# Optimization experiments

Hardware: AMD Instinct MI355X
Metric: run time of the kernel (lower is better)

The kernel has to match this reference:

```python
import jax, jax.numpy as jnp
import numpy as np

B, N, F_IN, F_OUT = 1, 8192, 256, 256
ALPHA = 0.2  # leaky relu negative slope
NEG_INF = -9e15


def setup_inputs() -> dict:
    key = jax.random.key(0)
    ks = jax.random.split(key, 8)
    feat = jax.random.normal(ks[0], (B, N, F_IN), dtype=jnp.float32)
    adj = jax.random.randint(ks[1], (B, N, N), 0, 2, dtype=jnp.int32)
    s = 1.414 * (6.0 / (F_IN + F_OUT)) ** 0.5
    W = jax.random.uniform(ks[2], (F_IN, F_OUT), minval=-s, maxval=s, dtype=jnp.float32)
    a_1 = jax.random.normal(ks[3], (F_OUT, 1), dtype=jnp.float32) * 0.1
    a_2 = jax.random.normal(ks[4], (F_OUT, 1), dtype=jnp.float32) * 0.1
    a_12 = jax.random.normal(ks[5], (F_OUT, F_OUT), dtype=jnp.float32) * (1.0 / F_OUT ** 0.5)
    W_1 = jax.random.uniform(ks[6], (F_IN, F_OUT), minval=-s, maxval=s, dtype=jnp.float32)
    W_2 = jax.random.uniform(ks[7], (F_IN, F_OUT), minval=-s, maxval=s, dtype=jnp.float32)
    return {"feat": feat, "adj": adj, "W": W, "a_1": a_1, "a_2": a_2,
            "a_12": a_12, "W_1": W_1, "W_2": W_2}


def reference(feat, adj, W, a_1, a_2, a_12, W_1, W_2):
    # --- attention logits ---
    h = jnp.matmul(feat, W)                       # [B,N,D]
    Ax = jnp.matmul(h, a_1)                       # [B,N,1]
    Ay = jnp.matmul(h, a_2)                       # [B,N,1]
    A_xy = jnp.matmul(jnp.matmul(h, a_12), jnp.swapaxes(h, 1, 2))  # [B,N,N]
    logits = jnp.swapaxes(Ax, 1, 2) + Ay + A_xy   # Ax^T broadcast over rows
    e = jax.nn.leaky_relu(logits, negative_slope=ALPHA)
    e = jnp.where(adj > 0, e, NEG_INF)
    attention = jax.nn.softmax(e, axis=-1)        # dropout is no-op (eval)
    # --- aggregate over RAW features ---
    h_prime = jnp.matmul(attention, feat)         # [B,N,F_IN]
    # --- dual linear update ---
    h_out = jnp.matmul(feat, W_1) + jnp.matmul(h_prime, W_2)
    return jax.nn.elu(h_out)
```

## Files before the change

kernel.cpp:

```cpp
#include <hip/hip_runtime.h>


typedef __attribute__((ext_vector_type(8))) _Float16 f16x8;
typedef __attribute__((ext_vector_type(4))) float f32x4;

#define NN 8192
#define DD 256
#define NSPLIT 4
#define NPART 4
#define CHUNK (NN / NSPLIT)
#define KVB 64
#define BM 32
#define NT (CHUNK / KVB)

#define MFMA16(a, b, c) __builtin_amdgcn_mfma_f32_16x16x32_f16(a, b, c, 0, 0, 0)
#define BAR_LGKM() asm volatile("s_waitcnt lgkmcnt(0)\n\ts_barrier" ::: "memory")
#define BAR_VM() asm volatile("s_waitcnt vmcnt(0)\n\ts_barrier" ::: "memory")

__device__ __forceinline__ short f2h(float f) {
  union { _Float16 h; short s; } u; u.h = (_Float16)f; return u.s;
}
__device__ __forceinline__ float h2f(short b) {
  union { short s; _Float16 h; } u; u.s = b; return (float)u.h;
}

typedef __attribute__((address_space(3))) unsigned lds_u32;
typedef const __attribute__((address_space(1))) unsigned glb_u32;
__device__ __forceinline__ void gl2lds16(const void* g, void* l) {
  __builtin_amdgcn_global_load_lds((glb_u32*)g, (lds_u32*)l, 16, 0, 0);
}

__global__ __launch_bounds__(256) void cvt_split_kernel(const float* __restrict__ in,
                                                        short* __restrict__ hi,
                                                        short* __restrict__ lo, int n) {
  for (int i = blockIdx.x * blockDim.x + threadIdx.x; i < n; i += gridDim.x * blockDim.x) {
    float f = in[i];
    short h = f2h(f);
    hi[i] = h;
    lo[i] = f2h(f - h2f(h));
  }
}

__global__ __launch_bounds__(256) void featT_kernel(const float* __restrict__ feat,
                                                    short* __restrict__ fT) {
  __shared__ float tile[32][33];
  const int i0 = blockIdx.x * 32, c0 = blockIdx.y * 32;
  const int r = threadIdx.x >> 5, c = threadIdx.x & 31;
#pragma unroll
  for (int p = 0; p < 4; ++p)
    tile[p * 8 + r][c] = feat[(size_t)(i0 + p * 8 + r) * DD + c0 + c];
  __syncthreads();
#pragma unroll
  for (int p = 0; p < 4; ++p)
    fT[(size_t)(c0 + p * 8 + r) * NN + i0 + c] = f2h(tile[c][p * 8 + r]);
}

__global__ __launch_bounds__(256) void transpose_split_kernel(const float* __restrict__ in,
                                                              short* __restrict__ tHi,
                                                              short* __restrict__ tLo) {
  int r = blockIdx.x, c = threadIdx.x;
  float f = in[r * DD + c];
  short h = f2h(f);
  tHi[c * DD + r] = h;
  if (tLo) tLo[c * DD + r] = f2h(f - h2f(h));
}

__global__ __launch_bounds__(256) void gemm_kernel(
    const short* __restrict__ Ahi, const short* __restrict__ Alo,
    const short* __restrict__ BThi, const short* __restrict__ BTlo,
    const short* __restrict__ A2, const short* __restrict__ BT2,
    short* __restrict__ outH, float* __restrict__ outF, int doElu) {
  const int lane = threadIdx.x & 63;
  const int w = threadIdx.x >> 6;
  const int l15 = lane & 15;
  const int koff = (lane >> 4) * 8;
  const int row0 = blockIdx.x * 64 + w * 16;
  const int col0 = blockIdx.y * 64;
  f32x4 acc[4] = {};
  const int aoff = (row0 + l15) * DD + koff;
#pragma unroll
  for (int kk = 0; kk < 8; ++kk) {
    f16x8 ah = *(const f16x8*)(Ahi + aoff + kk * 32);
#pragma unroll
    for (int cf = 0; cf < 4; ++cf) {
      int boff = (col0 + cf * 16 + l15) * DD + kk * 32 + koff;
      f16x8 bh = *(const f16x8*)(BThi + boff);
      acc[cf] = MFMA16(ah, bh, acc[cf]);
      if (Alo) {
        f16x8 al = *(const f16x8*)(Alo + aoff + kk * 32);
        acc[cf] = MFMA16(al, bh, acc[cf]);
      }
      if (BTlo) {
        f16x8 bl = *(const f16x8*)(BTlo + boff);
        acc[cf] = MFMA16(ah, bl, acc[cf]);
      }
    }
  }
  if (A2) {
#pragma unroll
    for (int kk = 0; kk < 8; ++kk) {
      f16x8 ah = *(const f16x8*)(A2 + aoff + kk * 32);
#pragma unroll
      for (int cf = 0; cf < 4; ++cf) {
        f16x8 bh = *(const f16x8*)(BT2 + (col0 + cf * 16 + l15) * DD + kk * 32 + koff);
        acc[cf] = MFMA16(ah, bh, acc[cf]);
      }
    }
  }
  const int crow = row0 + (lane >> 4) * 4;
#pragma unroll
  for (int cf = 0; cf < 4; ++cf) {
    int col = col0 + cf * 16 + l15;
#pragma unroll
    for (int r = 0; r < 4; ++r) {
      float v = acc[cf][r];
      if (doElu) v = (v > 0.f) ? v : expm1f(v);
      if (outF) outF[(crow + r) * DD + col] = v;
      if (outH) outH[(crow + r) * DD + col] = f2h(v);
    }
  }
}

__global__ __launch_bounds__(256) void axay_kernel(const short* __restrict__ hF,
                                                   const float* __restrict__ a1,
                                                   const float* __restrict__ a2,
                                                   float* __restrict__ ax,
                                                   float* __restrict__ ay) {
  const int lane = threadIdx.x & 63;
  const int w = threadIdx.x >> 6;
  const int row = blockIdx.x * 4 + w;
  float s1 = 0.f, s2 = 0.f;
#pragma unroll
  for (int j = 0; j < 4; ++j) {
    int k = lane * 4 + j;
    float hv = h2f(hF[row * DD + k]);
    s1 += hv * a1[k];
    s2 += hv * a2[k];
  }
#pragma unroll
  for (int m = 1; m < 64; m <<= 1) {
    s1 += __shfl_xor(s1, m);
    s2 += __shfl_xor(s2, m);
  }
  if (lane == 0) { ax[row] = s1; ay[row] = s2; }
}

__global__ __launch_bounds__(256, 2) void attn_kernel(
    const short* __restrict__ gF, const short* __restrict__ hF,
    const short* __restrict__ fT, const float* __restrict__ ax,
    const float* __restrict__ ay, const int* __restrict__ adj,
    short* __restrict__ numPart, float* __restrict__ mPart,
    float* __restrict__ lPart) {
  __shared__ short sG[BM * DD];
  __shared__ short sH[KVB * DD];
  __shared__ float sS[BM][68];
  __shared__ short sP[BM][80];
  __shared__ float sScale[BM];

  const int tid = threadIdx.x;
  const int lane = tid & 63;
  const int w = tid >> 6;
  const int wr = w >> 1, sp = w & 1;
  const int l15 = lane & 15;
  const int q0 = lane >> 4;
  const int crow = q0 * 4;

  const int bid = blockIdx.x;
  const int chunk = (bid & 7) >> 1;
  const int rowblk = ((bid >> 3) << 1) | (bid & 1);
  const int row0 = rowblk * BM;
  const int jbase = chunk * CHUNK;

  float ay4[4];
#pragma unroll
  for (int r = 0; r < 4; ++r) ay4[r] = ay[row0 + wr * 16 + crow + r];

#pragma unroll
  for (int R = 0; R < 4; ++R) {
    int dstb = R * 4096 + tid * 16;
    int lr = dstb >> 9;
    int srcb = (dstb & 511) ^ ((lr & 7) << 4);
    gl2lds16(gF + (row0 + lr) * DD + (srcb >> 1), (char*)sG + dstb);
  }
  auto stageH = [&](int jrow) {
#pragma unroll
    for (int R = 0; R < 8; ++R) {
      int dstb = R * 4096 + tid * 16;
      int lr = dstb >> 9;
      int srcb = (dstb & 511) ^ ((lr & 7) << 4);
      gl2lds16(hF + (jrow + lr) * DD + (srcb >> 1), (char*)sH + dstb);
    }
  };
  stageH(jbase);

  const size_t adjrow = (size_t)(row0 + wr * 16 + crow) * NN;
  int a8[2][4];
  float ax2[2];
#pragma unroll
  for (int cf = 0; cf < 2; ++cf) {
    int kb = jbase + sp * 32 + cf * 16 + l15;
#pragma unroll
    for (int r = 0; r < 4; ++r) a8[cf][r] = adj[adjrow + (size_t)r * NN + kb];
    ax2[cf] = ax[kb];
  }

  const int srow = tid >> 3;
  const int sc8 = (tid & 7) * 8;
  float m_run = -__builtin_inff();
  float l_run = 0.f;
  f32x4 accpv[2][4] = {};

  BAR_VM();

  for (int t = 0; t < NT; ++t) {
    const int j0 = jbase + t * KVB;
    f32x4 aA = {}, aB = {};
    {
      const int lrA = wr * 16 + l15;
      const int rbA = lrA * 512, swzA = (lrA & 7) << 4;
      const int lrB0 = sp * 32 + l15;
      const int rbB0 = lrB0 * 512, swzB0 = (lrB0 & 7) << 4;
      const int lrB1 = sp * 32 + 16 + l15;
      const int rbB1 = lrB1 * 512, swzB1 = (lrB1 & 7) << 4;
      __builtin_amdgcn_s_setprio(1);
#pragma unroll
      for (int kk = 0; kk < 8; ++kk) {
        const int slot = kk * 64 + q0 * 16;
        f16x8 ga = *(const f16x8*)((const char*)sG + rbA + (slot ^ swzA));
        f16x8 b0 = *(const f16x8*)((const char*)sH + rbB0 + (slot ^ swzB0));
        f16x8 b1 = *(const f16x8*)((const char*)sH + rbB1 + (slot ^ swzB1));
        aA = MFMA16(ga, b0, aA);
        aB = MFMA16(ga, b1, aB);
      }
      __builtin_amdgcn_s_setprio(0);
    }
#pragma unroll
    for (int cf = 0; cf < 2; ++cf) {
      const f32x4& ac = cf ? aB : aA;
#pragma unroll
      for (int r = 0; r < 4; ++r) {
        float v = ac[r] + ax2[cf] + ay4[r];
        v = (v > 0.f) ? v : 0.2f * v;
        sS[wr * 16 + crow + r][sp * 32 + cf * 16 + l15] =
            (a8[cf][r] > 0) ? v : -9.0e15f;
      }
    }
    BAR_LGKM();
    f16x8 vb[2][4];
#pragma unroll
    for (int ks = 0; ks < 2; ++ks)
#pragma unroll
      for (int df = 0; df < 4; ++df)
        vb[ks][df] = *(const f16x8*)(fT + (size_t)(w * 64 + df * 16 + l15) * NN +
                                     j0 + ks * 32 + q0 * 8);
    int a8n[2][4];
    float ax2n[2];
    {
      int jn = (t + 1 < NT) ? (j0 + KVB) : jbase;
#pragma unroll
      for (int cf = 0; cf < 2; ++cf) {
        int kb = jn + sp * 32 + cf * 16 + l15;
#pragma unroll
        for (int r = 0; r < 4; ++r) a8n[cf][r] = adj[adjrow + (size_t)r * NN + kb];
        ax2n[cf] = ax[kb];
      }
    }
    if (t + 1 < NT) stageH(j0 + KVB);
    {
      float4 s0 = *(const float4*)(&sS[srow][sc8]);
      float4 s1 = *(const float4*)(&sS[srow][sc8 + 4]);
      float tmax = fmaxf(fmaxf(fmaxf(s0.x, s0.y), fmaxf(s0.z, s0.w)),
                         fmaxf(fmaxf(s1.x, s1.y), fmaxf(s1.z, s1.w)));
      tmax = fmaxf(tmax, __shfl_xor(tmax, 1));
      tmax = fmaxf(tmax, __shfl_xor(tmax, 2));
      tmax = fmaxf(tmax, __shfl_xor(tmax, 4));
      float m_new = fmaxf(m_run, tmax);
      float scale = __expf(m_run - m_new);
      float p[8];
      p[0] = __expf(s0.x - m_new); p[1] = __expf(s0.y - m_new);
      p[2] = __expf(s0.z - m_new); p[3] = __expf(s0.w - m_new);
      p[4] = __expf(s1.x - m_new); p[5] = __expf(s1.y - m_new);
      p[6] = __expf(s1.z - m_new); p[7] = __expf(s1.w - m_new);
      float psum = ((p[0] + p[1]) + (p[2] + p[3])) + ((p[4] + p[5]) + (p[6] + p[7]));
      psum += __shfl_xor(psum, 1);
      psum += __shfl_xor(psum, 2);
      psum += __shfl_xor(psum, 4);
      l_run = l_run * scale + psum;
      m_run = m_new;
      union { short s[8]; f16x8 v; } pu;
#pragma unroll
      for (int c = 0; c < 8; ++c) pu.s[c] = f2h(p[c]);
      *(f16x8*)(&sP[srow][sc8]) = pu.v;
      if ((tid & 7) == 0) sScale[srow] = scale;
    }
    BAR_LGKM();
    {
      float4 sc0 = *(const float4*)(&sScale[crow]);
      float4 sc1 = *(const float4*)(&sScale[16 + crow]);
      const float* scp[2] = { &sc0.x, &sc1.x };
#pragma unroll
      for (int rg = 0; rg < 2; ++rg)
#pragma unroll
        for (int df = 0; df < 4; ++df)
#pragma unroll
          for (int r = 0; r < 4; ++r) accpv[rg][df][r] *= scp[rg][r];
      __builtin_amdgcn_s_setprio(1);
#pragma unroll
      for (int ks = 0; ks < 2; ++ks) {
        f16x8 pa0 = *(const f16x8*)(&sP[l15][ks * 32 + q0 * 8]);
        f16x8 pa1 = *(const f16x8*)(&sP[16 + l15][ks * 32 + q0 * 8]);
#pragma unroll
        for (int df = 0; df < 4; ++df) {
          accpv[0][df] = MFMA16(pa0, vb[ks][df], accpv[0][df]);
          accpv[1][df] = MFMA16(pa1, vb[ks][df], accpv[1][df]);
        }
      }
      __builtin_amdgcn_s_setprio(0);
    }
#pragma unroll
    for (int cf = 0; cf < 2; ++cf) {
#pragma unroll
      for (int r = 0; r < 4; ++r) a8[cf][r] = a8n[cf][r];
      ax2[cf] = ax2n[cf];
    }
    BAR_VM();
  }
  if ((tid & 7) == 0) {
    mPart[chunk * NN + row0 + srow] = m_run;
    lPart[chunk * NN + row0 + srow] = l_run;
  }
  short* np = numPart + (size_t)chunk * NN * DD;
#pragma unroll
  for (int rg = 0; rg < 2; ++rg)
#pragma unroll
    for (int df = 0; df < 4; ++df) {
      int col = w * 64 + df * 16 + l15;
#pragma unroll
      for (int r = 0; r < 4; ++r)
        np[(size_t)(row0 + rg * 16 + crow + r) * DD + col] = f2h(accpv[rg][df][r]);
    }
}

__global__ __launch_bounds__(256) void combine_kernel(
    const short* __restrict__ numPart, const float* __restrict__ mPart,
    const float* __restrict__ lPart, short* __restrict__ hp) {
  const int row = blockIdx.x;
  const int col = threadIdx.x;
  float m[NPART], l[NPART];
  float ms = -__builtin_inff();
#pragma unroll
  for (int i = 0; i < NPART; ++i) {
    m[i] = mPart[i * NN + row];
    l[i] = lPart[i * NN + row];
    ms = fmaxf(ms, m[i]);
  }
  float denom = 0.f, num = 0.f;
  const size_t idx = (size_t)row * DD + col;
#pragma unroll
  for (int i = 0; i < NPART; ++i) {
    float wgt = __expf(m[i] - ms);
    denom += l[i] * wgt;
    num += h2f(numPart[(size_t)i * NN * DD + idx]) * wgt;
  }
  hp[idx] = f2h(num / denom);
}

extern "C" void kernel_launch(void* const* d_in, const int* in_sizes, int n_in,
                              void* d_out, int out_size, void* d_ws, size_t ws_size,
                              hipStream_t stream) {
  const float* feat = (const float*)d_in[0];
  const int*   adj  = (const int*)d_in[1];
  const float* W    = (const float*)d_in[2];
  const float* a1   = (const float*)d_in[3];
  const float* a2   = (const float*)d_in[4];
  const float* a12  = (const float*)d_in[5];
  const float* W1   = (const float*)d_in[6];
  const float* W2   = (const float*)d_in[7];
  float* out = (float*)d_out;
  (void)in_sizes; (void)n_in; (void)out_size; (void)ws_size;

  char* ws = (char*)d_ws;
  size_t off = 0;
  auto alloc = [&](size_t b) { void* p = ws + off; off += (b + 255) & ~(size_t)255; return p; };
  short* featHi = (short*)alloc((size_t)NN * DD * 2);
  short* featLo = (short*)alloc((size_t)NN * DD * 2);
  short* fT     = (short*)alloc((size_t)NN * DD * 2);
  short* hF     = (short*)alloc((size_t)NN * DD * 2);
  short* gF     = (short*)alloc((size_t)NN * DD * 2);
  short* hp     = (short*)alloc((size_t)NN * DD * 2);
  short* WTh    = (short*)alloc((size_t)DD * DD * 2);
  short* WTl    = (short*)alloc((size_t)DD * DD * 2);
  short* A12Th  = (short*)alloc((size_t)DD * DD * 2);
  short* A12Tl  = (short*)alloc((size_t)DD * DD * 2);
  short* W1T    = (short*)alloc((size_t)DD * DD * 2);
  short* W2T    = (short*)alloc((size_t)DD * DD * 2);
  float* axv    = (float*)alloc((size_t)NN * 4);
  float* ayv    = (float*)alloc((size_t)NN * 4);
  short* numPart = (short*)alloc((size_t)NPART * NN * DD * 2);
  float* mPart   = (float*)alloc((size_t)NPART * NN * 4);
  float* lPart   = (float*)alloc((size_t)NPART * NN * 4);

  cvt_split_kernel<<<2048, 256, 0, stream>>>(feat, featHi, featLo, NN * DD);
  featT_kernel<<<dim3(NN / 32, DD / 32), 256, 0, stream>>>(feat, fT);
  transpose_split_kernel<<<DD, DD, 0, stream>>>(W, WTh, WTl);
  transpose_split_kernel<<<DD, DD, 0, stream>>>(a12, A12Th, A12Tl);
  transpose_split_kernel<<<DD, DD, 0, stream>>>(W1, W1T, nullptr);
  transpose_split_kernel<<<DD, DD, 0, stream>>>(W2, W2T, nullptr);
  gemm_kernel<<<dim3(NN / 64, DD / 64), 256, 0, stream>>>(
      featHi, featLo, WTh, WTl, nullptr, nullptr, hF, nullptr, 0);
  gemm_kernel<<<dim3(NN / 64, DD / 64), 256, 0, stream>>>(
      hF, nullptr, A12Th, A12Tl, nullptr, nullptr, gF, nullptr, 0);
  axay_kernel<<<NN / 4, 256, 0, stream>>>(hF, a1, a2, axv, ayv);
  attn_kernel<<<dim3((NN / BM) * NSPLIT), 256, 0, stream>>>(
      gF, hF, fT, axv, ayv, adj, numPart, mPart, lPart);
  combine_kernel<<<NN, DD, 0, stream>>>(numPart, mPart, lPart, hp);
  gemm_kernel<<<dim3(NN / 64, DD / 64), 256, 0, stream>>>(
      featHi, nullptr, W1T, nullptr, hp, W2T, nullptr, out, 1);
}
```

Before: 307.7 us.

## Keep softmax in registers per wave with deferred rescaling and per-wave partials

Moves the online softmax from a block-wide LDS score/probability exchange into per-wave registers. Each wave now owns its 16 rows and 32 key columns, keeps row max and sum per lane, and computes all 256 output columns, which removes one block barrier per tile and the sS/sScale buffers. The key range is split into 2 chunks instead of 4, and each chunk produces two wave-level partials (four in total). Partials are normalized by l before being stored as fp16, and the combine kernel reweights them by l. Rescaling is skipped while the new tile max stays within 8 of the running max, which trades register pressure (64 accumulator vectors) and more per-wave global V loads for fewer exp and multiply operations.

```diff
diff --git a/kernel.cpp b/kernel.cpp
--- a/kernel.cpp
+++ b/kernel.cpp
@@ -6,7 +6,7 @@
 
 #define NN 8192
 #define DD 256
-#define NSPLIT 4
+#define NSPLIT 2
 #define NPART 4
 #define CHUNK (NN / NSPLIT)
 #define KVB 64
@@ -153,9 +153,7 @@
     float* __restrict__ lPart) {
   __shared__ short sG[BM * DD];
   __shared__ short sH[KVB * DD];
-  __shared__ float sS[BM][68];
-  __shared__ short sP[BM][80];
-  __shared__ float sScale[BM];
+  __shared__ short sP[4][16][40];
 
   const int tid = threadIdx.x;
   const int lane = tid & 63;
@@ -163,17 +161,17 @@
   const int wr = w >> 1, sp = w & 1;
   const int l15 = lane & 15;
   const int q0 = lane >> 4;
-  const int crow = q0 * 4;
 
   const int bid = blockIdx.x;
-  const int chunk = (bid & 7) >> 1;
-  const int rowblk = ((bid >> 3) << 1) | (bid & 1);
+  const int chunk = (bid & 7) >> 2;
+  const int rowblk = (bid >> 3) * 4 + (bid & 3);
   const int row0 = rowblk * BM;
   const int jbase = chunk * CHUNK;
+  const int pidx = chunk * 2 + sp;
 
   float ay4[4];
 #pragma unroll
-  for (int r = 0; r < 4; ++r) ay4[r] = ay[row0 + wr * 16 + crow + r];
+  for (int r = 0; r < 4; ++r) ay4[r] = ay[row0 + wr * 16 + q0 * 4 + r];
 
 #pragma unroll
   for (int R = 0; R < 4; ++R) {
@@ -193,22 +191,21 @@
   };
   stageH(jbase);
 
-  const size_t adjrow = (size_t)(row0 + wr * 16 + crow) * NN;
+  const size_t adjb = (size_t)(row0 + wr * 16 + q0 * 4) * NN;
   int a8[2][4];
   float ax2[2];
 #pragma unroll
   for (int cf = 0; cf < 2; ++cf) {
     int kb = jbase + sp * 32 + cf * 16 + l15;
-#pragma unroll
-    for (int r = 0; r < 4; ++r) a8[cf][r] = adj[adjrow + (size_t)r * NN + kb];
     ax2[cf] = ax[kb];
-  }
-
-  const int srow = tid >> 3;
-  const int sc8 = (tid & 7) * 8;
-  float m_run = -__builtin_inff();
-  float l_run = 0.f;
-  f32x4 accpv[2][4] = {};
+#pragma unroll
+    for (int r = 0; r < 4; ++r) a8[cf][r] = adj[adjb + (size_t)r * NN + kb];
+  }
+
+  float m_run[4], l_run[4];
+#pragma unroll
+  for (int r = 0; r < 4; ++r) { m_run[r] = -__builtin_inff(); l_run[r] = 0.f; }
+  f32x4 accpv[16] = {};
 
   BAR_VM();
 
@@ -220,7 +217,7 @@
       const int rbA = lrA * 512, swzA = (lrA & 7) << 4;
       const int lrB0 = sp * 32 + l15;
       const int rbB0 = lrB0 * 512, swzB0 = (lrB0 & 7) << 4;
-      const int lrB1 = sp * 32 + 16 + l15;
+      const int lrB1 = lrB0 + 16;
       const int rbB1 = lrB1 * 512, swzB1 = (lrB1 & 7) << 4;
       __builtin_amdgcn_s_setprio(1);
 #pragma unroll
@@ -234,25 +231,8 @@
       }
       __builtin_amdgcn_s_setprio(0);
     }
-#pragma unroll
-    for (int cf = 0; cf < 2; ++cf) {
-      const f32x4& ac = cf ? aB : aA;
-#pragma unroll
-      for (int r = 0; r < 4; ++r) {
-        float v = ac[r] + ax2[cf] + ay4[r];
-        v = (v > 0.f) ? v : 0.2f * v;
-        sS[wr * 16 + crow + r][sp * 32 + cf * 16 + l15] =
-            (a8[cf][r] > 0) ? v : -9.0e15f;
-      }
-    }
     BAR_LGKM();
-    f16x8 vb[2][4];
-#pragma unroll
-    for (int ks = 0; ks < 2; ++ks)
-#pragma unroll
-      for (int df = 0; df < 4; ++df)
-        vb[ks][df] = *(const f16x8*)(fT + (size_t)(w * 64 + df * 16 + l15) * NN +
-                                     j0 + ks * 32 + q0 * 8);
+    if (t + 1 < NT) stageH(j0 + KVB);
     int a8n[2][4];
     float ax2n[2];
     {
@@ -260,63 +240,80 @@
 #pragma unroll
       for (int cf = 0; cf < 2; ++cf) {
         int kb = jn + sp * 32 + cf * 16 + l15;
-#pragma unroll
-        for (int r = 0; r < 4; ++r) a8n[cf][r] = adj[adjrow + (size_t)r * NN + kb];
         ax2n[cf] = ax[kb];
-      }
-    }
-    if (t + 1 < NT) stageH(j0 + KVB);
-    {
-      float4 s0 = *(const float4*)(&sS[srow][sc8]);
-      float4 s1 = *(const float4*)(&sS[srow][sc8 + 4]);
-      float tmax = fmaxf(fmaxf(fmaxf(s0.x, s0.y), fmaxf(s0.z, s0.w)),
-                         fmaxf(fmaxf(s1.x, s1.y), fmaxf(s1.z, s1.w)));
-      tmax = fmaxf(tmax, __shfl_xor(tmax, 1));
-      tmax = fmaxf(tmax, __shfl_xor(tmax, 2));
-      tmax = fmaxf(tmax, __shfl_xor(tmax, 4));
-      float m_new = fmaxf(m_run, tmax);
-      float scale = __expf(m_run - m_new);
-      float p[8];
-      p[0] = __expf(s0.x - m_new); p[1] = __expf(s0.y - m_new);
-      p[2] = __expf(s0.z - m_new); p[3] = __expf(s0.w - m_new);
-      p[4] = __expf(s1.x - m_new); p[5] = __expf(s1.y - m_new);
-      p[6] = __expf(s1.z - m_new); p[7] = __expf(s1.w - m_new);
-      float psum = ((p[0] + p[1]) + (p[2] + p[3])) + ((p[4] + p[5]) + (p[6] + p[7]));
-      psum += __shfl_xor(psum, 1);
-      psum += __shfl_xor(psum, 2);
-      psum += __shfl_xor(psum, 4);
-      l_run = l_run * scale + psum;
-      m_run = m_new;
-      union { short s[8]; f16x8 v; } pu;
-#pragma unroll
-      for (int c = 0; c < 8; ++c) pu.s[c] = f2h(p[c]);
-      *(f16x8*)(&sP[srow][sc8]) = pu.v;
-      if ((tid & 7) == 0) sScale[srow] = scale;
-    }
-    BAR_LGKM();
-    {
-      float4 sc0 = *(const float4*)(&sScale[crow]);
-      float4 sc1 = *(const float4*)(&sScale[16 + crow]);
-      const float* scp[2] = { &sc0.x, &sc1.x };
-#pragma unroll
-      for (int rg = 0; rg < 2; ++rg)
-#pragma unroll
-        for (int df = 0; df < 4; ++df)
-#pragma unroll
-          for (int r = 0; r < 4; ++r) accpv[rg][df][r] *= scp[rg][r];
-      __builtin_amdgcn_s_setprio(1);
-#pragma unroll
-      for (int ks = 0; ks < 2; ++ks) {
-        f16x8 pa0 = *(const f16x8*)(&sP[l15][ks * 32 + q0 * 8]);
-        f16x8 pa1 = *(const f16x8*)(&sP[16 + l15][ks * 32 + q0 * 8]);
-#pragma unroll
-        for (int df = 0; df < 4; ++df) {
-          accpv[0][df] = MFMA16(pa0, vb[ks][df], accpv[0][df]);
-          accpv[1][df] = MFMA16(pa1, vb[ks][df], accpv[1][df]);
-        }
-      }
-      __builtin_amdgcn_s_setprio(0);
-    }
+#pragma unroll
+        for (int r = 0; r < 4; ++r) a8n[cf][r] = adj[adjb + (size_t)r * NN + kb];
+      }
+    }
+    float s8[2][4];
+#pragma unroll
+    for (int cf = 0; cf < 2; ++cf)
+#pragma unroll
+      for (int r = 0; r < 4; ++r) {
+        float v = (cf ? aB[r] : aA[r]) + ax2[cf] + ay4[r];
+        v = (v > 0.f) ? v : 0.2f * v;
+        s8[cf][r] = (a8[cf][r] > 0) ? v : -9.0e15f;
+      }
+    float rowmax[4];
+#pragma unroll
+    for (int r = 0; r < 4; ++r) rowmax[r] = fmaxf(s8[0][r], s8[1][r]);
+#pragma unroll
+    for (int msk = 1; msk < 16; msk <<= 1)
+#pragma unroll
+      for (int r = 0; r < 4; ++r)
+        rowmax[r] = fmaxf(rowmax[r], __shfl_xor(rowmax[r], msk));
+    int cond = 1;
+#pragma unroll
+    for (int r = 0; r < 4; ++r) cond &= (rowmax[r] <= m_run[r] + 8.0f);
+    const int defer = __all(cond);
+    float scale[4];
+    if (defer) {
+#pragma unroll
+      for (int r = 0; r < 4; ++r) scale[r] = 1.0f;
+    } else {
+#pragma unroll
+      for (int r = 0; r < 4; ++r) {
+        float mn = fmaxf(m_run[r], rowmax[r]);
+        scale[r] = __expf(m_run[r] - mn);
+        m_run[r] = mn;
+      }
+    }
+    float psum[4] = {0.f, 0.f, 0.f, 0.f};
+    float p8[2][4];
+#pragma unroll
+    for (int cf = 0; cf < 2; ++cf)
+#pragma unroll
+      for (int r = 0; r < 4; ++r) {
+        float p = __expf(s8[cf][r] - m_run[r]);
+        p8[cf][r] = p;
+        psum[r] += p;
+      }
+#pragma unroll
+    for (int msk = 1; msk < 16; msk <<= 1)
+#pragma unroll
+      for (int r = 0; r < 4; ++r) psum[r] += __shfl_xor(psum[r], msk);
+#pragma unroll
+    for (int r = 0; r < 4; ++r) l_run[r] = l_run[r] * scale[r] + psum[r];
+#pragma unroll
+    for (int cf = 0; cf < 2; ++cf)
+#pragma unroll
+      for (int r = 0; r < 4; ++r)
+        sP[w][q0 * 4 + r][cf * 16 + l15] = f2h(p8[cf][r]);
+    f16x8 pa = *(const f16x8*)(&sP[w][l15][q0 * 8]);
+    if (!defer) {
+#pragma unroll
+      for (int df = 0; df < 16; ++df)
+#pragma unroll
+        for (int r = 0; r < 4; ++r) accpv[df][r] *= scale[r];
+    }
+    __builtin_amdgcn_s_setprio(1);
+#pragma unroll
+    for (int df = 0; df < 16; ++df) {
+      f16x8 vb = *(const f16x8*)(fT + (size_t)(df * 16 + l15) * NN +
+                                 j0 + sp * 32 + q0 * 8);
+      accpv[df] = MFMA16(pa, vb, accpv[df]);
+    }
+    __builtin_amdgcn_s_setprio(0);
 #pragma unroll
     for (int cf = 0; cf < 2; ++cf) {
 #pragma unroll
@@ -325,24 +322,28 @@
     }
     BAR_VM();
   }
-  if ((tid & 7) == 0) {
-    mPart[chunk * NN + row0 + srow] = m_run;
-    lPart[chunk * NN + row0 + srow] = l_run;
-  }
-  short* np = numPart + (size_t)chunk * NN * DD;
-#pragma unroll
-  for (int rg = 0; rg < 2; ++rg)
-#pragma unroll
-    for (int df = 0; df < 4; ++df) {
-      int col = w * 64 + df * 16 + l15;
-#pragma unroll
-      for (int r = 0; r < 4; ++r)
-        np[(size_t)(row0 + rg * 16 + crow + r) * DD + col] = f2h(accpv[rg][df][r]);
-    }
+  float inv[4];
+#pragma unroll
+  for (int r = 0; r < 4; ++r) inv[r] = 1.0f / l_run[r];
+  if (l15 == 0) {
+#pragma unroll
+    for (int r = 0; r < 4; ++r) {
+      int row = row0 + wr * 16 + q0 * 4 + r;
+      mPart[pidx * NN + row] = m_run[r];
+      lPart[pidx * NN + row] = l_run[r];
+    }
+  }
+  short* np = numPart + (size_t)pidx * NN * DD;
+#pragma unroll
+  for (int df = 0; df < 16; ++df)
+#pragma unroll
+    for (int r = 0; r < 4; ++r)
+      np[(size_t)(row0 + wr * 16 + q0 * 4 + r) * DD + df * 16 + l15] =
+          f2h(accpv[df][r] * inv[r]);
 }
 
 __global__ __launch_bounds__(256) void combine_kernel(
-    const short* __restrict__ numPart, const float* __restrict__ mPart,
+    const short* __restrict__ nbar, const float* __restrict__ mPart,
     const float* __restrict__ lPart, short* __restrict__ hp) {
   const int row = blockIdx.x;
   const int col = threadIdx.x;
@@ -358,9 +359,9 @@
   const size_t idx = (size_t)row * DD + col;
 #pragma unroll
   for (int i = 0; i < NPART; ++i) {
-    float wgt = __expf(m[i] - ms);
-    denom += l[i] * wgt;
-    num += h2f(numPart[(size_t)i * NN * DD + idx]) * wgt;
+    float wgt = __expf(m[i] - ms) * l[i];
+    denom += wgt;
+    num += h2f(nbar[(size_t)i * NN * DD + idx]) * wgt;
   }
   hp[idx] = f2h(num / denom);
 }
```

After: 446.0 us. 1.45x slower.

## Halve KV tile, double-buffer H in LDS, and reduce key-split count

Applied to the files above, without the earlier changes.

Shrinks the key tile from 64 to 32 and double-buffers the staged H tile in LDS, so the next tile's load is issued before the current tile's QK^T MFMAs. The V-tile, adjacency and ax loads are also moved to the top of the iteration to overlap with compute. The key-dimension split drops from 4 to 2 chunks, with the block-to-(chunk, rowblock) mapping changed to match. This cuts partial-result traffic and the cost of merging partials. In exchange it doubles the number of loop iterations, each with three barriers and less MFMA work. It also halves the grid-level parallelism from the split.

```diff
diff --git a/kernel.cpp b/kernel.cpp
--- a/kernel.cpp
+++ b/kernel.cpp
@@ -2,14 +2,15 @@
 
 
 typedef __attribute__((ext_vector_type(8))) _Float16 f16x8;
+typedef __attribute__((ext_vector_type(4))) short s16x4;
 typedef __attribute__((ext_vector_type(4))) float f32x4;
 
 #define NN 8192
 #define DD 256
-#define NSPLIT 4
-#define NPART 4
+#define NSPLIT 2
+#define NPART 2
 #define CHUNK (NN / NSPLIT)
-#define KVB 64
+#define KVB 32
 #define BM 32
 #define NT (CHUNK / KVB)
 
@@ -152,9 +153,9 @@
     short* __restrict__ numPart, float* __restrict__ mPart,
     float* __restrict__ lPart) {
   __shared__ short sG[BM * DD];
-  __shared__ short sH[KVB * DD];
-  __shared__ float sS[BM][68];
-  __shared__ short sP[BM][80];
+  __shared__ short sH[2][KVB * DD];
+  __shared__ float sS[BM][36];
+  __shared__ short sP[BM][40];
   __shared__ float sScale[BM];
 
   const int tid = threadIdx.x;
@@ -166,8 +167,8 @@
   const int crow = q0 * 4;
 
   const int bid = blockIdx.x;
-  const int chunk = (bid & 7) >> 1;
-  const int rowblk = ((bid >> 3) << 1) | (bid & 1);
+  const int chunk = (bid & 7) >> 2;
+  const int rowblk = (bid >> 3) * 4 + (bid & 3);
   const int row0 = rowblk * BM;
   const int jbase = chunk * CHUNK;
 
@@ -182,30 +183,29 @@
     int srcb = (dstb & 511) ^ ((lr & 7) << 4);
     gl2lds16(gF + (row0 + lr) * DD + (srcb >> 1), (char*)sG + dstb);
   }
-  auto stageH = [&](int jrow) {
-#pragma unroll
-    for (int R = 0; R < 8; ++R) {
+  auto stageH = [&](int buf, int jrow) {
+#pragma unroll
+    for (int R = 0; R < 4; ++R) {
       int dstb = R * 4096 + tid * 16;
       int lr = dstb >> 9;
       int srcb = (dstb & 511) ^ ((lr & 7) << 4);
-      gl2lds16(hF + (jrow + lr) * DD + (srcb >> 1), (char*)sH + dstb);
+      gl2lds16(hF + (jrow + lr) * DD + (srcb >> 1), (char*)sH[buf] + dstb);
     }
   };
-  stageH(jbase);
+  stageH(0, jbase);
 
   const size_t adjrow = (size_t)(row0 + wr * 16 + crow) * NN;
-  int a8[2][4];
-  float ax2[2];
-#pragma unroll
-  for (int cf = 0; cf < 2; ++cf) {
-    int kb = jbase + sp * 32 + cf * 16 + l15;
-#pragma unroll
-    for (int r = 0; r < 4; ++r) a8[cf][r] = adj[adjrow + (size_t)r * NN + kb];
-    ax2[cf] = ax[kb];
+  int a4[4];
+  float axv;
+  {
+    int kb = jbase + sp * 16 + l15;
+#pragma unroll
+    for (int r = 0; r < 4; ++r) a4[r] = adj[adjrow + (size_t)r * NN + kb];
+    axv = ax[kb];
   }
 
   const int srow = tid >> 3;
-  const int sc8 = (tid & 7) * 8;
+  const int sc4 = (tid & 7) * 4;
   float m_run = -__builtin_inff();
   float l_run = 0.f;
   f32x4 accpv[2][4] = {};
@@ -214,83 +214,63 @@
 
   for (int t = 0; t < NT; ++t) {
     const int j0 = jbase + t * KVB;
-    f32x4 aA = {}, aB = {};
+    f16x8 vb[4];
+#pragma unroll
+    for (int df = 0; df < 4; ++df)
+      vb[df] = *(const f16x8*)(fT + (size_t)(w * 64 + df * 16 + l15) * NN + j0 + q0 * 8);
+    int a4n[4];
+    float axn;
+    {
+      int jn = (t + 1 < NT) ? (j0 + KVB) : jbase;
+      int kb = jn + sp * 16 + l15;
+#pragma unroll
+      for (int r = 0; r < 4; ++r) a4n[r] = adj[adjrow + (size_t)r * NN + kb];
+      axn = ax[kb];
+    }
+    if (t + 1 < NT) stageH((t + 1) & 1, j0 + KVB);
+    f32x4 acc = {};
     {
       const int lrA = wr * 16 + l15;
       const int rbA = lrA * 512, swzA = (lrA & 7) << 4;
-      const int lrB0 = sp * 32 + l15;
-      const int rbB0 = lrB0 * 512, swzB0 = (lrB0 & 7) << 4;
-      const int lrB1 = sp * 32 + 16 + l15;
-      const int rbB1 = lrB1 * 512, swzB1 = (lrB1 & 7) << 4;
+      const int lrB = sp * 16 + l15;
+      const int rbB = lrB * 512, swzB = (lrB & 7) << 4;
+      const char* sHb = (const char*)sH[t & 1];
       __builtin_amdgcn_s_setprio(1);
 #pragma unroll
       for (int kk = 0; kk < 8; ++kk) {
         const int slot = kk * 64 + q0 * 16;
         f16x8 ga = *(const f16x8*)((const char*)sG + rbA + (slot ^ swzA));
-        f16x8 b0 = *(const f16x8*)((const char*)sH + rbB0 + (slot ^ swzB0));
-        f16x8 b1 = *(const f16x8*)((const char*)sH + rbB1 + (slot ^ swzB1));
-        aA = MFMA16(ga, b0, aA);
-        aB = MFMA16(ga, b1, aB);
+        f16x8 bh = *(const f16x8*)(sHb + rbB + (slot ^ swzB));
+        acc = MFMA16(ga, bh, acc);
       }
       __builtin_amdgcn_s_setprio(0);
     }
 #pragma unroll
-    for (int cf = 0; cf < 2; ++cf) {
-      const f32x4& ac = cf ? aB : aA;
-#pragma unroll
-      for (int r = 0; r < 4; ++r) {
-        float v = ac[r] + ax2[cf] + ay4[r];
-        v = (v > 0.f) ? v : 0.2f * v;
-        sS[wr * 16 + crow + r][sp * 32 + cf * 16 + l15] =
-            (a8[cf][r] > 0) ? v : -9.0e15f;
-      }
+    for (int r = 0; r < 4; ++r) {
+      float v = acc[r] + axv + ay4[r];
+      v = (v > 0.f) ? v : 0.2f * v;
+      sS[wr * 16 + crow + r][sp * 16 + l15] = (a4[r] > 0) ? v : -9.0e15f;
     }
     BAR_LGKM();
-    f16x8 vb[2][4];
-#pragma unroll
-    for (int ks = 0; ks < 2; ++ks)
-#pragma unroll
-      for (int df = 0; df < 4; ++df)
-        vb[ks][df] = *(const f16x8*)(fT + (size_t)(w * 64 + df * 16 + l15) * NN +
-                                     j0 + ks * 32 + q0 * 8);
-    int a8n[2][4];
-    float ax2n[2];
     {
-      int jn = (t + 1 < NT) ? (j0 + KVB) : jbase;
-#pragma unroll
-      for (int cf = 0; cf < 2; ++cf) {
-        int kb = jn + sp * 32 + cf * 16 + l15;
-#pragma unroll
-        for (int r = 0; r < 4; ++r) a8n[cf][r] = adj[adjrow + (size_t)r * NN + kb];
-        ax2n[cf] = ax[kb];
-      }
-    }
-    if (t + 1 < NT) stageH(j0 + KVB);
-    {
-      float4 s0 = *(const float4*)(&sS[srow][sc8]);
-      float4 s1 = *(const float4*)(&sS[srow][sc8 + 4]);
-      float tmax = fmaxf(fmaxf(fmaxf(s0.x, s0.y), fmaxf(s0.z, s0.w)),
-                         fmaxf(fmaxf(s1.x, s1.y), fmaxf(s1.z, s1.w)));
+      float4 sv = *(const float4*)(&sS[srow][sc4]);
+      float tmax = fmaxf(fmaxf(sv.x, sv.y), fmaxf(sv.z, sv.w));
       tmax = fmaxf(tmax, __shfl_xor(tmax, 1));
       tmax = fmaxf(tmax, __shfl_xor(tmax, 2));
       tmax = fmaxf(tmax, __shfl_xor(tmax, 4));
       float m_new = fmaxf(m_run, tmax);
       float scale = __expf(m_run - m_new);
-      float p[8];
-      p[0] = __expf(s0.x - m_new); p[1] = __expf(s0.y - m_new);
-      p[2] = __expf(s0.z - m_new); p[3] = __expf(s0.w - m_new);
-      p[4] = __expf(s1.x - m_new); p[5] = __expf(s1.y - m_new);
-      p[6] = __expf(s1.z - m_new); p[7] = __expf(s1.w - m_new);
-      float psum = ((p[0] + p[1]) + (p[2] + p[3])) + ((p[4] + p[5]) + (p[6] + p[7]));
+      float p0 = __expf(sv.x - m_new), p1 = __expf(sv.y - m_new);
+      float p2 = __expf(sv.z - m_new), p3 = __expf(sv.w - m_new);
+      float psum = (p0 + p1) + (p2 + p3);
       psum += __shfl_xor(psum, 1);
       psum += __shfl_xor(psum, 2);
       psum += __shfl_xor(psum, 4);
       l_run = l_run * scale + psum;
       m_run = m_new;
-      union { short s[8]; f16x8 v; } pu;
-#pragma unroll
-      for (int c = 0; c < 8; ++c) pu.s[c] = f2h(p[c]);
-      *(f16x8*)(&sP[srow][sc8]) = pu.v;
+      union { short s[4]; s16x4 v; } pu;
+      pu.s[0] = f2h(p0); pu.s[1] = f2h(p1); pu.s[2] = f2h(p2); pu.s[3] = f2h(p3);
+      *(s16x4*)(&sP[srow][sc4]) = pu.v;
       if ((tid & 7) == 0) sScale[srow] = scale;
     }
     BAR_LGKM();
@@ -304,25 +284,19 @@
         for (int df = 0; df < 4; ++df)
 #pragma unroll
           for (int r = 0; r < 4; ++r) accpv[rg][df][r] *= scp[rg][r];
+      f16x8 pa0 = *(const f16x8*)(&sP[l15][q0 * 8]);
+      f16x8 pa1 = *(const f16x8*)(&sP[16 + l15][q0 * 8]);
       __builtin_amdgcn_s_setprio(1);
 #pragma unroll
-      for (int ks = 0; ks < 2; ++ks) {
-        f16x8 pa0 = *(const f16x8*)(&sP[l15][ks * 32 + q0 * 8]);
-        f16x8 pa1 = *(const f16x8*)(&sP[16 + l15][ks * 32 + q0 * 8]);
-#pragma unroll
-        for (int df = 0; df < 4; ++df) {
-          accpv[0][df] = MFMA16(pa0, vb[ks][df], accpv[0][df]);
-          accpv[1][df] = MFMA16(pa1, vb[ks][df], accpv[1][df]);
-        }
+      for (int df = 0; df < 4; ++df) {
+        accpv[0][df] = MFMA16(pa0, vb[df], accpv[0][df]);
+        accpv[1][df] = MFMA16(pa1, vb[df], accpv[1][df]);
       }
       __builtin_amdgcn_s_setprio(0);
     }
 #pragma unroll
-    for (int cf = 0; cf < 2; ++cf) {
-#pragma unroll
-      for (int r = 0; r < 4; ++r) a8[cf][r] = a8n[cf][r];
-      ax2[cf] = ax2n[cf];
-    }
+    for (int r = 0; r < 4; ++r) a4[r] = a4n[r];
+    axv = axn;
     BAR_VM();
   }
   if ((tid & 7) == 0) {
```

New measurement: 352.9 us. 1.15x slower.

## Pack adjacency into bitmask and halve attention split count

Applied to the files above, without the earlier changes.

Adds a pre-pass that packs the int32 adjacency matrix into 32-bit bitmasks, so the attention kernel reads one word per row per 32 columns instead of one int per element. The key-range split drops from four to two chunks, which halves the partial numerator, max and sum buffers that combine must read. The pack kernel still reads the full 256 MB adjacency once, so the saving comes from cheaper per-tile mask loads and a smaller combine. The risk is fewer blocks in the attention launch (512 instead of 1024) and longer per-block loops.

```diff
diff --git a/kernel.cpp b/kernel.cpp
--- a/kernel.cpp
+++ b/kernel.cpp
@@ -6,12 +6,13 @@
 
 #define NN 8192
 #define DD 256
-#define NSPLIT 4
-#define NPART 4
+#define NSPLIT 2
+#define NPART 2
 #define CHUNK (NN / NSPLIT)
 #define KVB 64
 #define BM 32
 #define NT (CHUNK / KVB)
+#define NW (NN / 32)
 
 #define MFMA16(a, b, c) __builtin_amdgcn_mfma_f32_16x16x32_f16(a, b, c, 0, 0, 0)
 #define BAR_LGKM() asm volatile("s_waitcnt lgkmcnt(0)\n\ts_barrier" ::: "memory")
@@ -28,6 +29,22 @@
 typedef const __attribute__((address_space(1))) unsigned glb_u32;
 __device__ __forceinline__ void gl2lds16(const void* g, void* l) {
   __builtin_amdgcn_global_load_lds((glb_u32*)g, (lds_u32*)l, 16, 0, 0);
+}
+
+__global__ __launch_bounds__(256) void adjpack_kernel(const int* __restrict__ adj,
+                                                      unsigned* __restrict__ adjp) {
+  size_t wrd = (size_t)blockIdx.x * 256 + threadIdx.x;
+  const int* src = adj + wrd * 32;
+  unsigned m = 0;
+#pragma unroll
+  for (int i = 0; i < 32; i += 4) {
+    int4 v = *(const int4*)(src + i);
+    m |= (unsigned)(v.x > 0) << i;
+    m |= (unsigned)(v.y > 0) << (i + 1);
+    m |= (unsigned)(v.z > 0) << (i + 2);
+    m |= (unsigned)(v.w > 0) << (i + 3);
+  }
+  adjp[wrd] = m;
 }
 
 __global__ __launch_bounds__(256) void cvt_split_kernel(const float* __restrict__ in,
@@ -148,7 +165,7 @@
 __global__ __launch_bounds__(256, 2) void attn_kernel(
     const short* __restrict__ gF, const short* __restrict__ hF,
     const short* __restrict__ fT, const float* __restrict__ ax,
-    const float* __restrict__ ay, const int* __restrict__ adj,
+    const float* __restrict__ ay, const unsigned* __restrict__ adjp,
     short* __restrict__ numPart, float* __restrict__ mPart,
     float* __restrict__ lPart) {
   __shared__ short sG[BM * DD];
@@ -166,8 +183,8 @@
   const int crow = q0 * 4;
 
   const int bid = blockIdx.x;
-  const int chunk = (bid & 7) >> 1;
-  const int rowblk = ((bid >> 3) << 1) | (bid & 1);
+  const int chunk = (bid & 7) >> 2;
+  const int rowblk = (bid >> 3) * 4 + (bid & 3);
   const int row0 = rowblk * BM;
   const int jbase = chunk * CHUNK;
 
@@ -193,15 +210,15 @@
   };
   stageH(jbase);
 
-  const size_t adjrow = (size_t)(row0 + wr * 16 + crow) * NN;
-  int a8[2][4];
+  const size_t adjwb = (size_t)(row0 + wr * 16 + crow) * NW + sp;
+  unsigned aw[4];
   float ax2[2];
-#pragma unroll
-  for (int cf = 0; cf < 2; ++cf) {
-    int kb = jbase + sp * 32 + cf * 16 + l15;
-#pragma unroll
-    for (int r = 0; r < 4; ++r) a8[cf][r] = adj[adjrow + (size_t)r * NN + kb];
-    ax2[cf] = ax[kb];
+  {
+    int w0 = jbase >> 5;
+#pragma unroll
+    for (int r = 0; r < 4; ++r) aw[r] = adjp[adjwb + (size_t)r * NW + w0];
+#pragma unroll
+    for (int cf = 0; cf < 2; ++cf) ax2[cf] = ax[jbase + sp * 32 + cf * 16 + l15];
   }
 
   const int srow = tid >> 3;
@@ -237,12 +254,13 @@
 #pragma unroll
     for (int cf = 0; cf < 2; ++cf) {
       const f32x4& ac = cf ? aB : aA;
+      const int bit = cf * 16 + l15;
 #pragma unroll
       for (int r = 0; r < 4; ++r) {
         float v = ac[r] + ax2[cf] + ay4[r];
         v = (v > 0.f) ? v : 0.2f * v;
         sS[wr * 16 + crow + r][sp * 32 + cf * 16 + l15] =
-            (a8[cf][r] > 0) ? v : -9.0e15f;
+            ((aw[r] >> bit) & 1u) ? v : -9.0e15f;
       }
     }
     BAR_LGKM();
@@ -253,17 +271,15 @@
       for (int df = 0; df < 4; ++df)
         vb[ks][df] = *(const f16x8*)(fT + (size_t)(w * 64 + df * 16 + l15) * NN +
                                      j0 + ks * 32 + q0 * 8);
-    int a8n[2][4];
+    unsigned awn[4];
     float ax2n[2];
     {
       int jn = (t + 1 < NT) ? (j0 + KVB) : jbase;
-#pragma unroll
-      for (int cf = 0; cf < 2; ++cf) {
-        int kb = jn + sp * 32 + cf * 16 + l15;
-#pragma unroll
-        for (int r = 0; r < 4; ++r) a8n[cf][r] = adj[adjrow + (size_t)r * NN + kb];
-        ax2n[cf] = ax[kb];
-      }
+      int w0 = jn >> 5;
+#pragma unroll
+      for (int r = 0; r < 4; ++r) awn[r] = adjp[adjwb + (size_t)r * NW + w0];
+#pragma unroll
+      for (int cf = 0; cf < 2; ++cf) ax2n[cf] = ax[jn + sp * 32 + cf * 16 + l15];
     }
     if (t + 1 < NT) stageH(j0 + KVB);
     {
@@ -318,11 +334,8 @@
       __builtin_amdgcn_s_setprio(0);
     }
 #pragma unroll
-    for (int cf = 0; cf < 2; ++cf) {
-#pragma unroll
-      for (int r = 0; r < 4; ++r) a8[cf][r] = a8n[cf][r];
-      ax2[cf] = ax2n[cf];
-    }
+    for (int r = 0; r < 4; ++r) aw[r] = awn[r];
+    ax2[0] = ax2n[0]; ax2[1] = ax2n[1];
     BAR_VM();
   }
   if ((tid & 7) == 0) {
@@ -399,7 +412,9 @@
   short* numPart = (short*)alloc((size_t)NPART * NN * DD * 2);
   float* mPart   = (float*)alloc((size_t)NPART * NN * 4);
   float* lPart   = (float*)alloc((size_t)NPART * NN * 4);
-
+  unsigned* adjp = (unsigned*)alloc((size_t)NN * NW * 4);
+
+  adjpack_kernel<<<NN * NW / 256, 256, 0, stream>>>(adj, adjp);
   cvt_split_kernel<<<2048, 256, 0, stream>>>(feat, featHi, featLo, NN * DD);
   featT_kernel<<<dim3(NN / 32, DD / 32), 256, 0, stream>>>(feat, fT);
   transpose_split_kernel<<<DD, DD, 0, stream>>>(W, WTh, WTl);
@@ -412,7 +427,7 @@
       hF, nullptr, A12Th, A12Tl, nullptr, nullptr, gF, nullptr, 0);
   axay_kernel<<<NN / 4, 256, 0, stream>>>(hF, a1, a2, axv, ayv);
   attn_kernel<<<dim3((NN / BM) * NSPLIT), 256, 0, stream>>>(
-      gF, hF, fT, axv, ayv, adj, numPart, mPart, lPart);
+      gF, hF, fT, axv, ayv, adjp, numPart, mPart, lPart);
   combine_kernel<<<NN, DD, 0, stream>>>(numPart, mPart, lPart, hp);
   gemm_kernel<<<dim3(NN / 64, DD / 64), 256, 0, stream>>>(
       featHi, nullptr, W1T, nullptr, hp, W2T, nullptr, out, 1);
```

After: 335.7 us. +9.1%, slower.
